# Optimization experiments

Hardware: AMD Instinct MI355X
Metric: run time of the kernel (lower is better)

The kernel has to match this reference:

```python
import jax, jax.numpy as jnp
import numpy as np

N = 3000
NUM_CLASSES = 80
SIGMA = 0.5            # gaussian soft-NMS sigma (hardcoded 0.5 in forward)
SCORE_THRESHOLD = 0.05 # hardcoded 0.05 in forward


def setup_inputs() -> dict:
    key = jax.random.key(0)
    k1, k2, k3, k4 = jax.random.split(key, 4)
    # well-formed xyxy boxes: x2>x1, y2>y1
    xy = jax.random.uniform(k1, (N, 2), jnp.float32, 0.0, 1000.0)
    wh = jax.random.uniform(k2, (N, 2), jnp.float32, 10.0, 150.0)
    boxes = jnp.concatenate([xy, xy + wh], axis=1)          # [N,4]
    scores = jax.random.uniform(k3, (N,), jnp.float32)       # [N]
    idxs = jax.random.randint(k4, (N,), 0, NUM_CLASSES)      # [N] class ids
    return {"boxes": boxes, "scores": scores, "idxs": idxs}


def _iou_one_vs_all(box, boxes):
    # box [4], boxes [N,4] -> iou [N]
    x1 = jnp.maximum(box[0], boxes[:, 0])
    y1 = jnp.maximum(box[1], boxes[:, 1])
    x2 = jnp.minimum(box[2], boxes[:, 2])
    y2 = jnp.minimum(box[3], boxes[:, 3])
    inter = jnp.clip(x2 - x1, 0.0) * jnp.clip(y2 - y1, 0.0)
    area_a = (box[2] - box[0]) * (box[3] - box[1])
    area_b = (boxes[:, 2] - boxes[:, 0]) * (boxes[:, 3] - boxes[:, 1])
    return inter / (area_a + area_b - inter)


def _soft_nms(boxes, scores):
    # Sequential Gaussian soft-NMS. At step i: select remaining max-score box,
    # swap to slot i, decay all later scores by exp(-iou^2/sigma).
    n = boxes.shape[0]
    order = jnp.arange(n)
    rng = jnp.arange(n)

    def step(carry, i):
        b_s, s_s, ord_s = carry
        masked = jnp.where(rng < i, -jnp.inf, s_s)
        j = jnp.argmax(masked)
        # swap slots i and j in boxes / scores / order
        bi, bj = b_s[i], b_s[j]
        b_s = b_s.at[i].set(bj).at[j].set(bi)
        si, sj = s_s[i], s_s[j]
        s_s = s_s.at[i].set(sj).at[j].set(si)
        oi, oj = ord_s[i], ord_s[j]
        ord_s = ord_s.at[i].set(oj).at[j].set(oi)
        # gaussian decay of later boxes
        iou = _iou_one_vs_all(b_s[i], b_s)               # [N]
        decay = jnp.exp(-(iou * iou) / SIGMA)
        s_s = jnp.where(rng > i, s_s * decay, s_s)
        return (b_s, s_s, ord_s), None

    (b_s, s_s, ord_s), _ = jax.lax.scan(step, (boxes, scores, order), jnp.arange(n))
    return s_s, ord_s


def reference(boxes, scores, idxs):
    # batched trick: offset boxes per class so cross-class IoU is always 0
    max_coord = jnp.max(boxes)
    offsets = idxs.astype(boxes.dtype) * (max_coord + 1.0)   # [N]
    boxes_off = boxes + offsets[:, None]                     # [N,4]
    updated_scores, order = _soft_nms(boxes_off, scores)
    keep_mask = updated_scores > SCORE_THRESHOLD             # fixed-shape keep indicator
    return updated_scores, order, keep_mask
```

## Files before the change

### kernel.cpp

```cpp
#include <hip/hip_runtime.h>
#include <math.h>

#define NMAX 3008
#define CAPC 128
#define NCLS 80
#define IC   12
#define JC   16
#define JCH  192
#define RB   (IC*JC)

#define WS_DONE   0
#define WS_FSCORE 16
#define WS_RANKC  (WS_FSCORE + 4*NMAX)

__device__ __forceinline__ float wave_max64(float x) {
    int v;
    v = __float_as_int(x);
    x = fmaxf(x, __int_as_float(__builtin_amdgcn_update_dpp(v, v, 0x111, 0xf, 0xf, false)));
    v = __float_as_int(x);
    x = fmaxf(x, __int_as_float(__builtin_amdgcn_update_dpp(v, v, 0x112, 0xf, 0xf, false)));
    v = __float_as_int(x);
    x = fmaxf(x, __int_as_float(__builtin_amdgcn_update_dpp(v, v, 0x114, 0xf, 0xf, false)));
    v = __float_as_int(x);
    x = fmaxf(x, __int_as_float(__builtin_amdgcn_update_dpp(v, v, 0x118, 0xf, 0xf, false)));
    v = __float_as_int(x);
    x = fmaxf(x, __int_as_float(__builtin_amdgcn_update_dpp(v, v, 0x142, 0xa, 0xf, false)));
    v = __float_as_int(x);
    x = fmaxf(x, __int_as_float(__builtin_amdgcn_update_dpp(v, v, 0x143, 0xc, 0xf, false)));
    return __int_as_float(__builtin_amdgcn_readlane(__float_as_int(x), 63));
}

__global__ void __launch_bounds__(256)
nms_class_kernel(const float* __restrict__ boxes, const float* __restrict__ scores,
                 const int* __restrict__ idxs, char* __restrict__ ws, int n) {
#pragma clang fp contract(off)
    const int c = blockIdx.x;
    const int tid = threadIdx.x, wid = tid >> 6, lane = tid & 63;
    float* fscore = (float*)(ws + WS_FSCORE);
    unsigned long long* RANKC = (unsigned long long*)(ws + WS_RANKC);

    __shared__ int idxS[NMAX];
    __shared__ unsigned long long maskS[NMAX / 64];
    __shared__ float mx0[CAPC], mx1[CAPC], mx2[CAPC], mx3[CAPC], msc[CAPC];
    __shared__ unsigned short mgid[CAPC];
    __shared__ float D[64 * 64];
    __shared__ float redS[256];

    for (int i = c * 256 + tid; i < NMAX; i += NCLS * 256) RANKC[i] = 0ull;
    if (c == 0 && tid == 0) *(unsigned*)(ws + WS_DONE) = 0u;

    float m = -1e30f;
    for (int k = tid; k < n; k += 256) {
        idxS[k] = idxs[k];
        float4 bb = ((const float4*)boxes)[k];
        m = fmaxf(m, fmaxf(fmaxf(bb.x, bb.y), fmaxf(bb.z, bb.w)));
    }
    redS[tid] = m;
    __syncthreads();
    for (int s = 128; s > 0; s >>= 1) {
        if (tid < s) redS[tid] = fmaxf(redS[tid], redS[tid + s]);
        __syncthreads();
    }
    const float maxcp1 = redS[0] + 1.0f;
    const float off = (float)c * maxcp1;

    const int nch = (n + 63) / 64;
    for (int t = wid; t < nch; t += 4) {
        int k = t * 64 + lane;
        bool p = (k < n) && (idxS[k] == c);
        unsigned long long mk = __ballot(p);
        if (lane == 0) maskS[t] = mk;
    }
    __syncthreads();

    int run = 0;
    for (int t = 0; t < nch; t++) {
        unsigned long long mk = maskS[t];
        if ((t & 3) == wid) {
            if ((mk >> lane) & 1ull) {
                int pos = run + __popcll(mk & ((1ull << lane) - 1ull));
                if (pos < CAPC) {
                    int k = t * 64 + lane;
                    float4 bb = ((const float4*)boxes)[k];
                    mx0[pos] = bb.x + off; mx1[pos] = bb.y + off;
                    mx2[pos] = bb.z + off; mx3[pos] = bb.w + off;
                    msc[pos] = scores[k];
                    mgid[pos] = (unsigned short)k;
                }
            }
        }
        run += __popcll(mk);
    }
    const int cnt = run < CAPC ? run : CAPC;
    __syncthreads();

    if (cnt <= 64) {
        const bool v0 = lane < cnt;
        float c0 = 0, c1 = 0, c2 = 0, c3 = 0;
        if (v0) { c0 = mx0[lane]; c1 = mx1[lane]; c2 = mx2[lane]; c3 = mx3[lane]; }
        const float ab = (c2 - c0) * (c3 - c1);
        for (int i = wid; i < cnt; i += 4) {
            float w0 = mx0[i], w1 = mx1[i], w2 = mx2[i], w3 = mx3[i];
            float aw = (w2 - w0) * (w3 - w1);
            float x1 = fmaxf(w0, c0), y1 = fmaxf(w1, c1);
            float x2 = fminf(w2, c2), y2 = fminf(w3, c3);
            float iw = fmaxf(x2 - x1, 0.f), ih = fmaxf(y2 - y1, 0.f);
            float inter = iw * ih;
            float d = 1.0f;
            if (inter != 0.f) {
                float iou = inter / ((aw + ab) - inter);
                float arg = -(iou * iou) / 0.5f;
                d = (float)exp((double)arg);
            }
            D[i * 64 + lane] = d;
        }
        __syncthreads();

        if (wid == 0) {
            float sc = v0 ? msc[lane] : -1.f;
            int g = v0 ? mgid[lane] : 0;
            float frz = 0.f;
            for (int s = 0; s < cnt; s++) {
                float M = wave_max64(sc);
                int wm = __ffsll(__ballot(sc == M)) - 1;
                float d = D[wm * 64 + lane];
                if (lane == wm) { frz = M; sc = -1.f; }
                else if (sc >= 0.f) sc = sc * d;
            }
            if (v0) fscore[g] = frz;
        }
    } else if (wid == 0) {
        float sc0 = -1.f, sc1 = -1.f;
        float a0 = 0, a1 = 0, a2 = 0, a3 = 0, b0 = 0, b1 = 0, b2 = 0, b3 = 0;
        int g0 = 0, g1 = 0;
        if (lane < cnt) {
            sc0 = msc[lane];
            a0 = mx0[lane]; a1 = mx1[lane]; a2 = mx2[lane]; a3 = mx3[lane];
            g0 = mgid[lane];
        }
        if (64 + lane < cnt) {
            sc1 = msc[64 + lane];
            b0 = mx0[64 + lane]; b1 = mx1[64 + lane]; b2 = mx2[64 + lane]; b3 = mx3[64 + lane];
            g1 = mgid[64 + lane];
        }
        for (int s = 0; s < cnt; s++) {
            float M = fmaxf(sc0, sc1);
            for (int o = 32; o >= 1; o >>= 1) M = fmaxf(M, __shfl_xor(M, o, 64));
            unsigned long long balA = __ballot(sc0 == M);
            int wm;
            if (balA) wm = __ffsll(balA) - 1;
            else      wm = 64 + __ffsll(__ballot(sc1 == M)) - 1;
            float w0 = mx0[wm], w1 = mx1[wm], w2 = mx2[wm], w3 = mx3[wm];
            if (wm == lane)           { fscore[g0] = M; sc0 = -1.f; }
            else if (wm == 64 + lane) { fscore[g1] = M; sc1 = -1.f; }
            float area_w = (w2 - w0) * (w3 - w1);
            if (sc0 >= 0.f) {
                float x1 = fmaxf(w0, a0), y1 = fmaxf(w1, a1);
                float x2 = fminf(w2, a2), y2 = fminf(w3, a3);
                float iw = fmaxf(x2 - x1, 0.f), ih = fmaxf(y2 - y1, 0.f);
                float inter = iw * ih;
                float area_b = (a2 - a0) * (a3 - a1);
                float iou = inter / ((area_w + area_b) - inter);
                float arg = -(iou * iou) / 0.5f;
                sc0 = sc0 * (float)exp((double)arg);
            }
            if (sc1 >= 0.f) {
                float x1 = fmaxf(w0, b0), y1 = fmaxf(w1, b1);
                float x2 = fminf(w2, b2), y2 = fminf(w3, b3);
                float iw = fmaxf(x2 - x1, 0.f), ih = fmaxf(y2 - y1, 0.f);
                float inter = iw * ih;
                float area_b = (b2 - b0) * (b3 - b1);
                float iou = inter / ((area_w + area_b) - inter);
                float arg = -(iou * iou) / 0.5f;
                sc1 = sc1 * (float)exp((double)arg);
            }
        }
    }
}

__global__ void __launch_bounds__(256)
rank_finalize_kernel(char* __restrict__ ws, float* __restrict__ out, int n) {
    const int tid = threadIdx.x;
    float* fscore = (float*)(ws + WS_FSCORE);
    unsigned long long* RANKC = (unsigned long long*)(ws + WS_RANKC);
    unsigned* done = (unsigned*)(ws + WS_DONE);

    __shared__ float sv[JCH];

    const int bx = blockIdx.x % IC;
    const int by = blockIdx.x / IC;
    const int chunk = (n + JC - 1) / JC;
    const int j0 = by * chunk;
    const int jn = min(n - j0, chunk);
    for (int j = tid; j < jn; j += 256) sv[j] = fscore[j0 + j];
    __syncthreads();

    int i = bx * 256 + tid;
    if (i < n) {
        float s = fscore[i];
        int gt = 0, eq = 0, eqlt = 0;
        for (int jj = 0; jj < jn; jj++) {
            float x = sv[jj];
            gt   += (x > s) ? 1 : 0;
            eq   += (x == s) ? 1 : 0;
            eqlt += (x == s && (j0 + jj) < i) ? 1 : 0;
        }
        unsigned long long packed = (unsigned long long)(unsigned)gt
                                  | ((unsigned long long)(unsigned)eqlt << 16)
                                  | ((unsigned long long)(unsigned)eq << 32);
        atomicAdd(&RANKC[i], packed);
    }
    __syncthreads();
    __threadfence();

    __shared__ int lastS;
    if (tid == 0) lastS = (atomicAdd(done, 1u) == RB - 1);
    __syncthreads();
    if (!lastS) return;

    __shared__ unsigned short ordL[NMAX];
    __shared__ float          svL[NMAX];
    __shared__ unsigned short slotL[NMAX];
    __shared__ unsigned short batL[NMAX];
    __shared__ unsigned char  tieL[NMAX];
    __shared__ int rstopS;
    if (tid == 0) rstopS = 0;
    __syncthreads();

    for (int b = tid; b < n; b += 256) {
        unsigned long long p = atomicAdd(&RANKC[b], 0ull);
        unsigned gt   = (unsigned)(p & 0xffffu);
        unsigned eqlt = (unsigned)((p >> 16) & 0xffffu);
        unsigned eq   = (unsigned)((p >> 32) & 0xffffu);
        int r = (int)(gt + eqlt);
        ordL[r] = (unsigned short)b;
        svL[r] = fscore[b];
        slotL[b] = (unsigned short)b;
        batL[b]  = (unsigned short)b;
        if (eq >= 2 && (unsigned)b < gt) atomicMax(&rstopS, (int)(gt + eq));
    }
    __syncthreads();

    for (int r = tid; r < n; r += 256)
        tieL[r] = (r + 1 < n) && (svL[r] == svL[r + 1]);
    __syncthreads();

    if (rstopS > 0 && tid == 0) {
        const int rstop = rstopS;
        int r = 0;
        while (r < rstop) {
            if (!tieL[r]) {
                int w = ordL[r];
                int j = slotL[w];
                int d = batL[r];
                batL[j] = (unsigned short)d;
                slotL[d] = (unsigned short)j;
                r++;
            } else {
                int g = 1;
                while (tieL[r + g - 1]) g++;
                for (int t = 0; t < g; t++) {
                    int bi = r + t;
                    int bs = slotL[ordL[bi]];
                    for (int q = r + t + 1; q < r + g; q++) {
                        int s2 = slotL[ordL[q]];
                        if (s2 < bs) { bs = s2; bi = q; }
                    }
                    unsigned short w = ordL[bi];
                    ordL[bi] = ordL[r + t];
                    ordL[r + t] = w;
                    int d = batL[r + t];
                    batL[bs] = (unsigned short)d;
                    slotL[d] = (unsigned short)bs;
                }
                r += g;
            }
        }
    }
    __syncthreads();

    for (int r = tid; r < n; r += 256) {
        float s = svL[r];
        out[r] = s;
        out[n + r] = (float)ordL[r];
        out[2 * n + r] = (s > 0.05f) ? 1.f : 0.f;
    }
}

extern "C" void kernel_launch(void* const* d_in, const int* in_sizes, int n_in,
                              void* d_out, int out_size, void* d_ws, size_t ws_size,
                              hipStream_t stream) {
    const float* boxes  = (const float*)d_in[0];
    const float* scores = (const float*)d_in[1];
    const int*   idxs   = (const int*)d_in[2];
    float* out = (float*)d_out;
    char* ws = (char*)d_ws;
    const int n = in_sizes[1];

    nms_class_kernel<<<NCLS, 256, 0, stream>>>(boxes, scores, idxs, ws, n);
    rank_finalize_kernel<<<RB, 256, 0, stream>>>(ws, out, n);
}
```

Before: 101.8 us.

## Fuse NMS and rank kernels into one cooperative launch with grid syncs

Merges the per-class soft-NMS kernel and the rank/finalize kernel into a single cooperative kernel of 192 blocks. Grid-wide barriers replace the second launch and the last-block atomic counter. Rank partials are now written per chunk into a 10-bit packed array instead of being accumulated with 64-bit atomics, and block 0 sums them. This removes one kernel launch and the workspace zeroing, but adds two grid syncs and cooperative-launch overhead.

```diff
diff --git a/kernel.cpp b/kernel.cpp
--- a/kernel.cpp
+++ b/kernel.cpp
@@ -1,5 +1,8 @@
 #include <hip/hip_runtime.h>
+#include <hip/hip_cooperative_groups.h>
 #include <math.h>
+
+namespace cg = cooperative_groups;
 
 #define NMAX 3008
 #define CAPC 128
@@ -7,11 +10,10 @@
 #define IC   12
 #define JC   16
 #define JCH  192
-#define RB   (IC*JC)
-
-#define WS_DONE   0
-#define WS_FSCORE 16
-#define WS_RANKC  (WS_FSCORE + 4*NMAX)
+#define GRID (IC*JC)
+
+#define WS_FSCORE 0
+#define WS_PART   (4*NMAX)
 
 __device__ __forceinline__ float wave_max64(float x) {
     int v;
@@ -31,13 +33,14 @@
 }
 
 __global__ void __launch_bounds__(256)
-nms_class_kernel(const float* __restrict__ boxes, const float* __restrict__ scores,
-                 const int* __restrict__ idxs, char* __restrict__ ws, int n) {
+fused_nms_kernel(const float* __restrict__ boxes, const float* __restrict__ scores,
+                 const int* __restrict__ idxs, char* __restrict__ ws,
+                 float* __restrict__ out, int n) {
 #pragma clang fp contract(off)
-    const int c = blockIdx.x;
+    cg::grid_group grid = cg::this_grid();
     const int tid = threadIdx.x, wid = tid >> 6, lane = tid & 63;
     float* fscore = (float*)(ws + WS_FSCORE);
-    unsigned long long* RANKC = (unsigned long long*)(ws + WS_RANKC);
+    unsigned* PART = (unsigned*)(ws + WS_PART);
 
     __shared__ int idxS[NMAX];
     __shared__ unsigned long long maskS[NMAX / 64];
@@ -45,193 +48,185 @@
     __shared__ unsigned short mgid[CAPC];
     __shared__ float D[64 * 64];
     __shared__ float redS[256];
-
-    for (int i = c * 256 + tid; i < NMAX; i += NCLS * 256) RANKC[i] = 0ull;
-    if (c == 0 && tid == 0) *(unsigned*)(ws + WS_DONE) = 0u;
-
-    float m = -1e30f;
-    for (int k = tid; k < n; k += 256) {
-        idxS[k] = idxs[k];
-        float4 bb = ((const float4*)boxes)[k];
-        m = fmaxf(m, fmaxf(fmaxf(bb.x, bb.y), fmaxf(bb.z, bb.w)));
-    }
-    redS[tid] = m;
-    __syncthreads();
-    for (int s = 128; s > 0; s >>= 1) {
-        if (tid < s) redS[tid] = fmaxf(redS[tid], redS[tid + s]);
-        __syncthreads();
-    }
-    const float maxcp1 = redS[0] + 1.0f;
-    const float off = (float)c * maxcp1;
-
-    const int nch = (n + 63) / 64;
-    for (int t = wid; t < nch; t += 4) {
-        int k = t * 64 + lane;
-        bool p = (k < n) && (idxS[k] == c);
-        unsigned long long mk = __ballot(p);
-        if (lane == 0) maskS[t] = mk;
-    }
-    __syncthreads();
-
-    int run = 0;
-    for (int t = 0; t < nch; t++) {
-        unsigned long long mk = maskS[t];
-        if ((t & 3) == wid) {
-            if ((mk >> lane) & 1ull) {
-                int pos = run + __popcll(mk & ((1ull << lane) - 1ull));
-                if (pos < CAPC) {
-                    int k = t * 64 + lane;
-                    float4 bb = ((const float4*)boxes)[k];
-                    mx0[pos] = bb.x + off; mx1[pos] = bb.y + off;
-                    mx2[pos] = bb.z + off; mx3[pos] = bb.w + off;
-                    msc[pos] = scores[k];
-                    mgid[pos] = (unsigned short)k;
-                }
-            }
-        }
-        run += __popcll(mk);
-    }
-    const int cnt = run < CAPC ? run : CAPC;
-    __syncthreads();
-
-    if (cnt <= 64) {
-        const bool v0 = lane < cnt;
-        float c0 = 0, c1 = 0, c2 = 0, c3 = 0;
-        if (v0) { c0 = mx0[lane]; c1 = mx1[lane]; c2 = mx2[lane]; c3 = mx3[lane]; }
-        const float ab = (c2 - c0) * (c3 - c1);
-        for (int i = wid; i < cnt; i += 4) {
-            float w0 = mx0[i], w1 = mx1[i], w2 = mx2[i], w3 = mx3[i];
-            float aw = (w2 - w0) * (w3 - w1);
-            float x1 = fmaxf(w0, c0), y1 = fmaxf(w1, c1);
-            float x2 = fminf(w2, c2), y2 = fminf(w3, c3);
-            float iw = fmaxf(x2 - x1, 0.f), ih = fmaxf(y2 - y1, 0.f);
-            float inter = iw * ih;
-            float d = 1.0f;
-            if (inter != 0.f) {
-                float iou = inter / ((aw + ab) - inter);
-                float arg = -(iou * iou) / 0.5f;
-                d = (float)exp((double)arg);
-            }
-            D[i * 64 + lane] = d;
-        }
-        __syncthreads();
-
-        if (wid == 0) {
-            float sc = v0 ? msc[lane] : -1.f;
-            int g = v0 ? mgid[lane] : 0;
-            float frz = 0.f;
-            for (int s = 0; s < cnt; s++) {
-                float M = wave_max64(sc);
-                int wm = __ffsll(__ballot(sc == M)) - 1;
-                float d = D[wm * 64 + lane];
-                if (lane == wm) { frz = M; sc = -1.f; }
-                else if (sc >= 0.f) sc = sc * d;
-            }
-            if (v0) fscore[g] = frz;
-        }
-    } else if (wid == 0) {
-        float sc0 = -1.f, sc1 = -1.f;
-        float a0 = 0, a1 = 0, a2 = 0, a3 = 0, b0 = 0, b1 = 0, b2 = 0, b3 = 0;
-        int g0 = 0, g1 = 0;
-        if (lane < cnt) {
-            sc0 = msc[lane];
-            a0 = mx0[lane]; a1 = mx1[lane]; a2 = mx2[lane]; a3 = mx3[lane];
-            g0 = mgid[lane];
-        }
-        if (64 + lane < cnt) {
-            sc1 = msc[64 + lane];
-            b0 = mx0[64 + lane]; b1 = mx1[64 + lane]; b2 = mx2[64 + lane]; b3 = mx3[64 + lane];
-            g1 = mgid[64 + lane];
-        }
-        for (int s = 0; s < cnt; s++) {
-            float M = fmaxf(sc0, sc1);
-            for (int o = 32; o >= 1; o >>= 1) M = fmaxf(M, __shfl_xor(M, o, 64));
-            unsigned long long balA = __ballot(sc0 == M);
-            int wm;
-            if (balA) wm = __ffsll(balA) - 1;
-            else      wm = 64 + __ffsll(__ballot(sc1 == M)) - 1;
-            float w0 = mx0[wm], w1 = mx1[wm], w2 = mx2[wm], w3 = mx3[wm];
-            if (wm == lane)           { fscore[g0] = M; sc0 = -1.f; }
-            else if (wm == 64 + lane) { fscore[g1] = M; sc1 = -1.f; }
-            float area_w = (w2 - w0) * (w3 - w1);
-            if (sc0 >= 0.f) {
-                float x1 = fmaxf(w0, a0), y1 = fmaxf(w1, a1);
-                float x2 = fminf(w2, a2), y2 = fminf(w3, a3);
-                float iw = fmaxf(x2 - x1, 0.f), ih = fmaxf(y2 - y1, 0.f);
-                float inter = iw * ih;
-                float area_b = (a2 - a0) * (a3 - a1);
-                float iou = inter / ((area_w + area_b) - inter);
-                float arg = -(iou * iou) / 0.5f;
-                sc0 = sc0 * (float)exp((double)arg);
-            }
-            if (sc1 >= 0.f) {
-                float x1 = fmaxf(w0, b0), y1 = fmaxf(w1, b1);
-                float x2 = fminf(w2, b2), y2 = fminf(w3, b3);
-                float iw = fmaxf(x2 - x1, 0.f), ih = fmaxf(y2 - y1, 0.f);
-                float inter = iw * ih;
-                float area_b = (b2 - b0) * (b3 - b1);
-                float iou = inter / ((area_w + area_b) - inter);
-                float arg = -(iou * iou) / 0.5f;
-                sc1 = sc1 * (float)exp((double)arg);
-            }
-        }
-    }
-}
-
-__global__ void __launch_bounds__(256)
-rank_finalize_kernel(char* __restrict__ ws, float* __restrict__ out, int n) {
-    const int tid = threadIdx.x;
-    float* fscore = (float*)(ws + WS_FSCORE);
-    unsigned long long* RANKC = (unsigned long long*)(ws + WS_RANKC);
-    unsigned* done = (unsigned*)(ws + WS_DONE);
-
     __shared__ float sv[JCH];
-
-    const int bx = blockIdx.x % IC;
-    const int by = blockIdx.x / IC;
-    const int chunk = (n + JC - 1) / JC;
-    const int j0 = by * chunk;
-    const int jn = min(n - j0, chunk);
-    for (int j = tid; j < jn; j += 256) sv[j] = fscore[j0 + j];
-    __syncthreads();
-
-    int i = bx * 256 + tid;
-    if (i < n) {
-        float s = fscore[i];
-        int gt = 0, eq = 0, eqlt = 0;
-        for (int jj = 0; jj < jn; jj++) {
-            float x = sv[jj];
-            gt   += (x > s) ? 1 : 0;
-            eq   += (x == s) ? 1 : 0;
-            eqlt += (x == s && (j0 + jj) < i) ? 1 : 0;
-        }
-        unsigned long long packed = (unsigned long long)(unsigned)gt
-                                  | ((unsigned long long)(unsigned)eqlt << 16)
-                                  | ((unsigned long long)(unsigned)eq << 32);
-        atomicAdd(&RANKC[i], packed);
-    }
-    __syncthreads();
-    __threadfence();
-
-    __shared__ int lastS;
-    if (tid == 0) lastS = (atomicAdd(done, 1u) == RB - 1);
-    __syncthreads();
-    if (!lastS) return;
-
     __shared__ unsigned short ordL[NMAX];
     __shared__ float          svL[NMAX];
     __shared__ unsigned short slotL[NMAX];
     __shared__ unsigned short batL[NMAX];
     __shared__ unsigned char  tieL[NMAX];
     __shared__ int rstopS;
+
+    const int c = blockIdx.x;
+    if (c < NCLS) {
+        float m = -1e30f;
+        for (int k = tid; k < n; k += 256) {
+            idxS[k] = idxs[k];
+            float4 bb = ((const float4*)boxes)[k];
+            m = fmaxf(m, fmaxf(fmaxf(bb.x, bb.y), fmaxf(bb.z, bb.w)));
+        }
+        redS[tid] = m;
+        __syncthreads();
+        for (int s = 128; s > 0; s >>= 1) {
+            if (tid < s) redS[tid] = fmaxf(redS[tid], redS[tid + s]);
+            __syncthreads();
+        }
+        const float maxcp1 = redS[0] + 1.0f;
+        const float off = (float)c * maxcp1;
+
+        const int nch = (n + 63) / 64;
+        for (int t = wid; t < nch; t += 4) {
+            int k = t * 64 + lane;
+            bool p = (k < n) && (idxS[k] == c);
+            unsigned long long mk = __ballot(p);
+            if (lane == 0) maskS[t] = mk;
+        }
+        __syncthreads();
+
+        int run = 0;
+        for (int t = 0; t < nch; t++) {
+            unsigned long long mk = maskS[t];
+            if ((t & 3) == wid) {
+                if ((mk >> lane) & 1ull) {
+                    int pos = run + __popcll(mk & ((1ull << lane) - 1ull));
+                    if (pos < CAPC) {
+                        int k = t * 64 + lane;
+                        float4 bb = ((const float4*)boxes)[k];
+                        mx0[pos] = bb.x + off; mx1[pos] = bb.y + off;
+                        mx2[pos] = bb.z + off; mx3[pos] = bb.w + off;
+                        msc[pos] = scores[k];
+                        mgid[pos] = (unsigned short)k;
+                    }
+                }
+            }
+            run += __popcll(mk);
+        }
+        const int cnt = run < CAPC ? run : CAPC;
+        __syncthreads();
+
+        if (cnt <= 64) {
+            const bool v0 = lane < cnt;
+            float c0 = 0, c1 = 0, c2 = 0, c3 = 0;
+            if (v0) { c0 = mx0[lane]; c1 = mx1[lane]; c2 = mx2[lane]; c3 = mx3[lane]; }
+            const float ab = (c2 - c0) * (c3 - c1);
+            for (int i = wid; i < cnt; i += 4) {
+                float w0 = mx0[i], w1 = mx1[i], w2 = mx2[i], w3 = mx3[i];
+                float aw = (w2 - w0) * (w3 - w1);
+                float x1 = fmaxf(w0, c0), y1 = fmaxf(w1, c1);
+                float x2 = fminf(w2, c2), y2 = fminf(w3, c3);
+                float iw = fmaxf(x2 - x1, 0.f), ih = fmaxf(y2 - y1, 0.f);
+                float inter = iw * ih;
+                float d = 1.0f;
+                if (inter != 0.f) {
+                    float iou = inter / ((aw + ab) - inter);
+                    float arg = -(iou * iou) / 0.5f;
+                    d = (float)exp((double)arg);
+                }
+                D[i * 64 + lane] = d;
+            }
+            __syncthreads();
+
+            if (wid == 0) {
+                float sc = v0 ? msc[lane] : -1.f;
+                int g = v0 ? mgid[lane] : 0;
+                float frz = 0.f;
+                for (int s = 0; s < cnt; s++) {
+                    float M = wave_max64(sc);
+                    int wm = __ffsll(__ballot(sc == M)) - 1;
+                    float d = D[wm * 64 + lane];
+                    if (lane == wm) { frz = M; sc = -1.f; }
+                    else if (sc >= 0.f) sc = sc * d;
+                }
+                if (v0) fscore[g] = frz;
+            }
+        } else if (wid == 0) {
+            float sc0 = -1.f, sc1 = -1.f;
+            float a0 = 0, a1 = 0, a2 = 0, a3 = 0, b0 = 0, b1 = 0, b2 = 0, b3 = 0;
+            int g0 = 0, g1 = 0;
+            if (lane < cnt) {
+                sc0 = msc[lane];
+                a0 = mx0[lane]; a1 = mx1[lane]; a2 = mx2[lane]; a3 = mx3[lane];
+                g0 = mgid[lane];
+            }
+            if (64 + lane < cnt) {
+                sc1 = msc[64 + lane];
+                b0 = mx0[64 + lane]; b1 = mx1[64 + lane]; b2 = mx2[64 + lane]; b3 = mx3[64 + lane];
+                g1 = mgid[64 + lane];
+            }
+            for (int s = 0; s < cnt; s++) {
+                float M = fmaxf(sc0, sc1);
+                for (int o = 32; o >= 1; o >>= 1) M = fmaxf(M, __shfl_xor(M, o, 64));
+                unsigned long long balA = __ballot(sc0 == M);
+                int wm;
+                if (balA) wm = __ffsll(balA) - 1;
+                else      wm = 64 + __ffsll(__ballot(sc1 == M)) - 1;
+                float w0 = mx0[wm], w1 = mx1[wm], w2 = mx2[wm], w3 = mx3[wm];
+                if (wm == lane)           { fscore[g0] = M; sc0 = -1.f; }
+                else if (wm == 64 + lane) { fscore[g1] = M; sc1 = -1.f; }
+                float area_w = (w2 - w0) * (w3 - w1);
+                if (sc0 >= 0.f) {
+                    float x1 = fmaxf(w0, a0), y1 = fmaxf(w1, a1);
+                    float x2 = fminf(w2, a2), y2 = fminf(w3, a3);
+                    float iw = fmaxf(x2 - x1, 0.f), ih = fmaxf(y2 - y1, 0.f);
+                    float inter = iw * ih;
+                    float area_b = (a2 - a0) * (a3 - a1);
+                    float iou = inter / ((area_w + area_b) - inter);
+                    float arg = -(iou * iou) / 0.5f;
+                    sc0 = sc0 * (float)exp((double)arg);
+                }
+                if (sc1 >= 0.f) {
+                    float x1 = fmaxf(w0, b0), y1 = fmaxf(w1, b1);
+                    float x2 = fminf(w2, b2), y2 = fminf(w3, b3);
+                    float iw = fmaxf(x2 - x1, 0.f), ih = fmaxf(y2 - y1, 0.f);
+                    float inter = iw * ih;
+                    float area_b = (b2 - b0) * (b3 - b1);
+                    float iou = inter / ((area_w + area_b) - inter);
+                    float arg = -(iou * iou) / 0.5f;
+                    sc1 = sc1 * (float)exp((double)arg);
+                }
+            }
+        }
+    }
+
+    grid.sync();
+
+    {
+        const int bx = blockIdx.x % IC;
+        const int by = blockIdx.x / IC;
+        const int chunk = (n + JC - 1) / JC;
+        const int j0 = by * chunk;
+        const int jn = min(n - j0, chunk);
+        for (int j = tid; j < jn; j += 256) sv[j] = fscore[j0 + j];
+        __syncthreads();
+
+        int i = bx * 256 + tid;
+        if (i < n) {
+            float s = fscore[i];
+            int gt = 0, eq = 0, eqlt = 0;
+            for (int jj = 0; jj < jn; jj++) {
+                float x = sv[jj];
+                gt   += (x > s) ? 1 : 0;
+                eq   += (x == s) ? 1 : 0;
+                eqlt += (x == s && (j0 + jj) < i) ? 1 : 0;
+            }
+            PART[by * NMAX + i] = (unsigned)gt | ((unsigned)eqlt << 10) | ((unsigned)eq << 20);
+        }
+    }
+
+    grid.sync();
+
+    if (blockIdx.x != 0) return;
     if (tid == 0) rstopS = 0;
     __syncthreads();
 
     for (int b = tid; b < n; b += 256) {
-        unsigned long long p = atomicAdd(&RANKC[b], 0ull);
-        unsigned gt   = (unsigned)(p & 0xffffu);
-        unsigned eqlt = (unsigned)((p >> 16) & 0xffffu);
-        unsigned eq   = (unsigned)((p >> 32) & 0xffffu);
+        unsigned gt = 0, eqlt = 0, eq = 0;
+#pragma unroll
+        for (int jc = 0; jc < JC; jc++) {
+            unsigned p = PART[jc * NMAX + b];
+            gt   += p & 1023u;
+            eqlt += (p >> 10) & 1023u;
+            eq   += (p >> 20) & 1023u;
+        }
         int r = (int)(gt + eqlt);
         ordL[r] = (unsigned short)b;
         svL[r] = fscore[b];
@@ -295,8 +290,10 @@
     const int*   idxs   = (const int*)d_in[2];
     float* out = (float*)d_out;
     char* ws = (char*)d_ws;
-    const int n = in_sizes[1];
-
-    nms_class_kernel<<<NCLS, 256, 0, stream>>>(boxes, scores, idxs, ws, n);
-    rank_finalize_kernel<<<RB, 256, 0, stream>>>(ws, out, n);
+    int n = in_sizes[1];
+
+    void* args[] = { (void*)&boxes, (void*)&scores, (void*)&idxs,
+                     (void*)&ws, (void*)&out, (void*)&n };
+    hipLaunchCooperativeKernel((const void*)fused_nms_kernel,
+                               dim3(GRID), dim3(256), args, 0, stream);
 }
```

New measurement: 143.2 us. 1.41x slower.
